# Optimization experiments

Measured on AMD Instinct MI355X. Metric: run time of the kernel, lower is better.

## Reference

```python
import jax, jax.numpy as jnp
import numpy as np

NUM_POINTS = 4
MAX_LEVELS = 2


def _bilinear(img, gx, gy, align_corners):
    # img: [C,H,W]; gx,gy: [P] normalized coords in [-1,1]; zero padding (torch grid_sample)
    C, H, W = img.shape
    if align_corners:
        ix = (gx + 1.0) * 0.5 * (W - 1)
        iy = (gy + 1.0) * 0.5 * (H - 1)
    else:
        ix = ((gx + 1.0) * W - 1.0) * 0.5
        iy = ((gy + 1.0) * H - 1.0) * 0.5
    x0 = jnp.floor(ix)
    y0 = jnp.floor(iy)
    wx1 = ix - x0
    wy1 = iy - y0

    def corner(xf, yf, w):
        xi = xf.astype(jnp.int32)
        yi = yf.astype(jnp.int32)
        valid = (xi >= 0) & (xi < W) & (yi >= 0) & (yi < H)
        v = img[:, jnp.clip(yi, 0, H - 1), jnp.clip(xi, 0, W - 1)]  # [C,P]
        return v * (w * valid)[None, :]

    return (corner(x0, y0, (1 - wx1) * (1 - wy1))
            + corner(x0 + 1, y0, wx1 * (1 - wy1))
            + corner(x0, y0 + 1, (1 - wx1) * wy1)
            + corner(x0 + 1, y0 + 1, wx1 * wy1))


_sample_ac = jax.vmap(lambda im, a, b: _bilinear(im, a, b, True))   # warp_affine path
_sample = jax.vmap(lambda im, a, b: _bilinear(im, a, b, False))     # MSDeformAttn path


def _warp_affine(src, M):
    # torch F.affine_grid + F.grid_sample, align_corners=True; src [N,C,H,W], M [N,2,3]
    N, C, H, W = src.shape
    ys = jnp.linspace(-1.0, 1.0, H)
    xs = jnp.linspace(-1.0, 1.0, W)
    gy, gx = jnp.meshgrid(ys, xs, indexing='ij')
    base = jnp.stack([gx.ravel(), gy.ravel(), jnp.ones(H * W, src.dtype)], 0)  # [3,HW]
    grid = jnp.einsum('nij,jp->nip', M, base)  # [N,2,HW]
    return _sample_ac(src, grid[:, 0], grid[:, 1]).reshape(N, C, H, W)


def setup_inputs() -> dict:
    key = jax.random.key(0)
    k = jax.random.split(key, 6)
    B, C, H, W = 2, 256, 100, 252
    x = jax.random.normal(k[0], (4, C, H, W), jnp.float32)
    record_len = jnp.full((B,), 2, dtype=jnp.int32)
    eye = jnp.array([[1.0, 0.0, 0.0], [0.0, 1.0, 0.0]], jnp.float32)
    pairwise_t_matrix = eye + 0.05 * jax.random.normal(k[1], (B, 2, 2, 2, 3), jnp.float32)
    w_off = 0.02 * jax.random.normal(k[2], (C, MAX_LEVELS * NUM_POINTS * 2), jnp.float32)
    b_off = 0.01 * jax.random.normal(k[3], (MAX_LEVELS * NUM_POINTS * 2,), jnp.float32)
    w_attn = 0.02 * jax.random.normal(k[4], (C, MAX_LEVELS * NUM_POINTS), jnp.float32)
    b_attn = 0.01 * jax.random.normal(k[5], (MAX_LEVELS * NUM_POINTS,), jnp.float32)
    return {"x": x, "record_len": record_len, "pairwise_t_matrix": pairwise_t_matrix,
            "w_off": w_off, "b_off": b_off, "w_attn": w_attn, "b_attn": b_attn}


def reference(x, record_len, pairwise_t_matrix, w_off, b_off, w_attn, b_attn):
    rl = [int(v) for v in np.asarray(record_len)]
    C, H, W = x.shape[1:]
    HW = H * W
    # get_reference_points(dim='2d'): pixel centers normalized to (0,1)
    rx = (jnp.arange(W, dtype=x.dtype) + 0.5) / W
    ry = (jnp.arange(H, dtype=x.dtype) + 0.5) / H
    gy, gx = jnp.meshgrid(ry, rx, indexing='ij')
    ref = jnp.stack([gx.ravel(), gy.ravel()], -1)  # [HW,2]
    norm = jnp.array([W, H], dtype=x.dtype)  # offset_normalizer = (W,H) per level
    outs = []
    start = 0
    for b, n in enumerate(rl):
        xx = x[start:start + n]
        start += n
        warped = _warp_affine(xx, pairwise_t_matrix[b, 0, :n])  # [n,C,H,W]
        q = warped[0].reshape(C, HW).T  # query = first agent, [HW,C]
        off = (q @ w_off + b_off).reshape(HW, MAX_LEVELS, NUM_POINTS, 2)[:, :n]  # [HW,n,P,2]
        aw = (q @ w_attn + b_attn).reshape(HW, MAX_LEVELS, NUM_POINTS)[:, :n]
        aw = jax.nn.softmax(aw.reshape(HW, n * NUM_POINTS), axis=-1).reshape(HW, n, NUM_POINTS)
        loc = ref[:, None, None, :] + off / norm  # sampling locations in (0,1)
        grid = 2.0 * loc - 1.0  # [HW,n,P,2]
        gxs = grid[..., 0].transpose(1, 0, 2).reshape(n, HW * NUM_POINTS)
        gys = grid[..., 1].transpose(1, 0, 2).reshape(n, HW * NUM_POINTS)
        sampled = _sample(warped, gxs, gys).reshape(n, C, HW, NUM_POINTS)
        out = jnp.einsum('lcqp,qlp->cq', sampled, aw)  # weighted sum over levels*points
        outs.append(out.reshape(1, C, H, W))
    return jnp.concatenate(outs, 0)
```

## Files before the change

### kernel.cpp

```cpp
#include <hip/hip_runtime.h>
#include <stdint.h>

#define CCH 256
#define NCP 128
#define HH  100
#define WW  252
#define HWSZ (HH*WW)
#define NIMG 4
#define NB   2
#define LP   8

#define TW 64
#define TH 4
#define HLO 2
#define PAIRS_BLOCK 16
#define TILESX ((WW + TW - 1)/TW)
#define TILESY (HH/TH)

#define WRW 70
#define WRH 5
#define WPL 384
#define WISS 6

typedef float vf2 __attribute__((ext_vector_type(2)));

__device__ __forceinline__ uint32_t f2bf(float a) {
  uint32_t u = __float_as_uint(a);
  u += 0x7fffu + ((u >> 16) & 1u);
  return u >> 16;
}
__device__ __forceinline__ float lof(uint32_t u) {
  return __uint_as_float(u << 16);
}
__device__ __forceinline__ float hif(uint32_t u) {
  return __uint_as_float(u & 0xffff0000u);
}
__device__ __forceinline__ vf2 unpk(uint32_t u) {
  vf2 r; r.x = lof(u); r.y = hif(u); return r;
}

__device__ __forceinline__ int swzN(int bid, int N) {
  int xcd = bid & 7, idx = bid >> 3;
  int q = N >> 3, r = N & 7;
  return (xcd < r) ? xcd*(q+1) + idx : r*(q+1) + (xcd-r)*q + idx;
}

__device__ __forceinline__ void gload_lds_u(const uint32_t* g, uint32_t* l) {
  auto gp = reinterpret_cast<const uint32_t __attribute__((address_space(1)))*>(
      reinterpret_cast<uintptr_t>(g));
  auto lp = reinterpret_cast<uint32_t __attribute__((address_space(3)))*>(
      reinterpret_cast<uintptr_t>(l));
  __builtin_amdgcn_global_load_lds(gp, lp, 4, 0, 0);
}

struct RowCtx {
  float w0, w1, w2, w3;
  uint32_t vt, vb;
  bool cnd;
};

__global__ __launch_bounds__(256) void warp_kernel(
    const float* __restrict__ x, const float* __restrict__ tmat,
    uint32_t* __restrict__ wpk)
{
  int tid = threadIdx.x;
  int ybase = 2*swzN(blockIdx.x, HH/2);
  int g  = blockIdx.y;
  int cc = blockIdx.z;
  bool valid = tid < WW;
  int xo = min(tid, WW-1);
  int b = g >> 1, i = g & 1;
  const float* M = tmat + (size_t)(b*4 + i)*6;
  float m00=M[0], m01=M[1], m02=M[2], m10=M[3], m11=M[4], m12=M[5];
  float gx = -1.0f + 2.0f*(float)xo/(float)(WW-1);

  RowCtx c0, c1;
  #pragma unroll
  for (int r = 0; r < 2; ++r) {
    int y = ybase + r;
    float gy = -1.0f + 2.0f*(float)y/(float)(HH-1);
    float sx = m00*gx + m01*gy + m02;
    float sy = m10*gx + m11*gy + m12;
    float ix = (sx + 1.0f)*0.5f*(float)(WW-1);
    float iy = (sy + 1.0f)*0.5f*(float)(HH-1);
    float x0f = floorf(ix), y0f = floorf(iy);
    float wx1 = ix - x0f,  wy1 = iy - y0f;
    int x0 = (int)x0f, y0 = (int)y0f;
    int x1 = x0 + 1,  y1 = y0 + 1;
    float v0x = (x0 >= 0 && x0 < WW) ? 1.f : 0.f;
    float v1x = (x1 >= 0 && x1 < WW) ? 1.f : 0.f;
    float v0y = (y0 >= 0 && y0 < HH) ? 1.f : 0.f;
    float v1y = (y1 >= 0 && y1 < HH) ? 1.f : 0.f;
    RowCtx c;
    c.w0 = (1.f-wx1)*(1.f-wy1)*v0x*v0y;
    c.w1 = wx1*(1.f-wy1)*v1x*v0y;
    c.w2 = (1.f-wx1)*wy1*v0x*v1y;
    c.w3 = wx1*wy1*v1x*v1y;
    int yc0 = min(max(y0,0),HH-1), yc1 = min(max(y1,0),HH-1);
    int xb  = min(max(x0,0),WW-2);
    c.cnd = (x0 == xb);
    c.vt = (uint32_t)(yc0*WW + xb)*4u;
    c.vb = (uint32_t)(yc1*WW + xb)*4u;
    if (r == 0) c0 = c; else c1 = c;
  }

  const float* src = x + ((size_t)g*CCH + (size_t)cc*32)*HWSZ;
  uint32_t* dst0 = wpk + ((size_t)g*NCP + (size_t)cc*PAIRS_BLOCK)*HWSZ
                   + ybase*WW + xo;
  uint32_t* dst1 = dst0 + WW;

  vf2 d[4][4];

  #define WLDQ(q) do {                                                       \
    const RowCtx& C = ((q)&1) ? c1 : c0;                                     \
    uint32_t co = (uint32_t)(2*((q)>>1))*(HWSZ*4u);                          \
    asm volatile("global_load_dwordx2 %0, %1, %2"                            \
      : "=v"(d[(q)&3][0]) : "v"(C.vt + co), "s"(src));                       \
    asm volatile("global_load_dwordx2 %0, %1, %2"                            \
      : "=v"(d[(q)&3][1]) : "v"(C.vb + co), "s"(src));                       \
    asm volatile("global_load_dwordx2 %0, %1, %2"                            \
      : "=v"(d[(q)&3][2]) : "v"(C.vt + co + HWSZ*4u), "s"(src));             \
    asm volatile("global_load_dwordx2 %0, %1, %2"                            \
      : "=v"(d[(q)&3][3]) : "v"(C.vb + co + HWSZ*4u), "s"(src));             \
  } while (0)

  #define WCPQ(q) do {                                                       \
    const RowCtx& C = ((q)&1) ? c1 : c0;                                     \
    uint32_t* D = ((q)&1) ? dst1 : dst0;                                     \
    vf2 t0 = d[(q)&3][0], b0 = d[(q)&3][1];                                  \
    vf2 t1 = d[(q)&3][2], b1 = d[(q)&3][3];                                  \
    float va0 = C.cnd ? t0.x : t0.y, vb0 = C.cnd ? t0.y : t0.x;              \
    float vc0 = C.cnd ? b0.x : b0.y, vd0 = C.cnd ? b0.y : b0.x;              \
    float va1 = C.cnd ? t1.x : t1.y, vb1 = C.cnd ? t1.y : t1.x;              \
    float vc1 = C.cnd ? b1.x : b1.y, vd1 = C.cnd ? b1.y : b1.x;              \
    float v0 = va0*C.w0 + vb0*C.w1 + vc0*C.w2 + vd0*C.w3;                    \
    float v1 = va1*C.w0 + vb1*C.w1 + vc1*C.w2 + vd1*C.w3;                    \
    if (valid) D[(size_t)((q)>>1)*HWSZ] = f2bf(v0) | (f2bf(v1) << 16);       \
  } while (0)

  WLDQ(0); WLDQ(1); WLDQ(2); WLDQ(3);
  #pragma unroll
  for (int q = 0; q < 2*PAIRS_BLOCK; ++q) {
    if      (q == 0)  { asm volatile("s_waitcnt vmcnt(12)" ::: "memory"); }
    else if (q == 1)  { asm volatile("s_waitcnt vmcnt(13)" ::: "memory"); }
    else if (q == 2)  { asm volatile("s_waitcnt vmcnt(14)" ::: "memory"); }
    else if (q <= 28) { asm volatile("s_waitcnt vmcnt(15)" ::: "memory"); }
    else if (q == 29) { asm volatile("s_waitcnt vmcnt(11)" ::: "memory"); }
    else if (q == 30) { asm volatile("s_waitcnt vmcnt(7)"  ::: "memory"); }
    else              { asm volatile("s_waitcnt vmcnt(3)"  ::: "memory"); }
    __builtin_amdgcn_sched_barrier(0);
    WCPQ(q);
    if (q + 4 < 2*PAIRS_BLOCK) WLDQ(q + 4);
  }
  #undef WLDQ
  #undef WCPQ
}

__global__ __launch_bounds__(256) void b1_kernel(
    const uint32_t* __restrict__ wpk,
    const float* __restrict__ w_off,  const float* __restrict__ b_off,
    const float* __restrict__ w_attn, const float* __restrict__ b_attn,
    float* __restrict__ taps)
{
  __shared__ float red[3][64][25];
  int tid   = threadIdx.x;
  int lpx   = tid & 63;
  int slice = tid >> 6;
  int pix   = blockIdx.x * 64 + lpx;
  int b     = blockIdx.y;
  bool valid = pix < HWSZ;
  int pxc = valid ? pix : (HWSZ-1);
  const uint32_t* q = wpk + ((size_t)(2*b)*NCP + (size_t)slice*32)*HWSZ + pxc;
  float acc[24];
  #pragma unroll
  for (int j=0;j<24;++j) acc[j] = 0.f;
  for (int cp=0; cp<32; ++cp) {
    uint32_t u = q[(size_t)cp*HWSZ];
    float qlo = lof(u), qhi = hif(u);
    int cg = slice*64 + 2*cp;
    #pragma unroll
    for (int j=0;j<16;++j) acc[j]    += qlo * w_off[cg*16+j]  + qhi * w_off[(cg+1)*16+j];
    #pragma unroll
    for (int j=0;j<8;++j)  acc[16+j] += qlo * w_attn[cg*8+j]  + qhi * w_attn[(cg+1)*8+j];
  }
  if (slice > 0) {
    #pragma unroll
    for (int j=0;j<24;++j) red[slice-1][lpx][j] = acc[j];
  }
  __syncthreads();
  if (slice == 0 && valid) {
    #pragma unroll
    for (int s=0;s<3;++s)
      #pragma unroll
      for (int j=0;j<24;++j) acc[j] += red[s][lpx][j];
    #pragma unroll
    for (int j=0;j<16;++j) acc[j]    += b_off[j];
    #pragma unroll
    for (int j=0;j<8;++j)  acc[16+j] += b_attn[j];
    float m = acc[16];
    #pragma unroll
    for (int j=1;j<8;++j) m = fmaxf(m, acc[16+j]);
    float e[8]; float s = 0.f;
    #pragma unroll
    for (int j=0;j<8;++j){ e[j] = __expf(acc[16+j]-m); s += e[j]; }
    float inv = 1.0f/s;
    int px = pix % WW, py = pix / WW;
    float* t = taps + (size_t)b*24*HWSZ + pix;
    #pragma unroll
    for (int k=0;k<LP;++k) {
      t[(size_t)k*HWSZ]      = (float)px + acc[2*k];
      t[(size_t)(8+k)*HWSZ]  = (float)py + acc[2*k+1];
      t[(size_t)(16+k)*HWSZ] = e[k]*inv;
    }
  }
}

__global__ __launch_bounds__(256) void b2_kernel(
    const uint32_t* __restrict__ wpk, const float* __restrict__ taps,
    float* __restrict__ out)
{
  __shared__ uint32_t lds[4*2*2*WPL];
  int tid  = threadIdx.x;
  int lane = tid & 63, wid = tid >> 6;
  int s100 = swzN(blockIdx.x, TILESX*TILESY);
  int tx   = s100 / TILESY;
  int ty   = s100 - tx*TILESY;
  int b    = blockIdx.y;
  int pbase = blockIdx.z * PAIRS_BLOCK;
  int tx0 = tx * TW;
  int ty0 = ty * TH;
  int px = tx0 + lane;
  int py = ty0 + wid;
  bool valid = (px < WW);
  int pxc = min(px, WW-1);
  int pix = py*WW + pxc;
  int cx0 = tx0 - HLO;
  int ry0 = py - HLO;

  const float* t = taps + (size_t)b*24*HWSZ + pix;
  float wgt[LP][4];
  int   lidx[LP];
  bool fastall = true;
  #pragma unroll
  for (int k=0;k<LP;++k) {
    float ix = t[(size_t)k*HWSZ];
    float iy = t[(size_t)(8+k)*HWSZ];
    float aw = t[(size_t)(16+k)*HWSZ];
    float x0f = floorf(ix), y0f = floorf(iy);
    float wx1 = ix-x0f, wy1 = iy-y0f;
    int x0=(int)x0f, y0=(int)y0f;
    float v0x = (x0   >= 0 && x0   < WW) ? 1.f : 0.f;
    float v1x = (x0+1 >= 0 && x0+1 < WW) ? 1.f : 0.f;
    float v0y = (y0   >= 0 && y0   < HH) ? 1.f : 0.f;
    float v1y = (y0+1 >= 0 && y0+1 < HH) ? 1.f : 0.f;
    wgt[k][0] = (1.f-wx1)*(1.f-wy1)*v0x*v0y*aw;
    wgt[k][1] = wx1*(1.f-wy1)*v1x*v0y*aw;
    wgt[k][2] = (1.f-wx1)*wy1*v0x*v1y*aw;
    wgt[k][3] = wx1*wy1*v1x*v1y*aw;
    bool f = (x0 >= cx0) && (x0 <= cx0+WRW-2) && (y0 >= ry0) && (y0 <= ry0+WRH-2);
    fastall = fastall && f;
    int li = (y0-ry0)*WRW + (x0-cx0);
    lidx[k] = f ? li : 0;
  }

  int goff[WISS];
  #pragma unroll
  for (int n=0;n<WISS;++n) {
    int e = n*64 + lane;
    int r = e / WRW;
    int c = e - r*WRW;
    int gy = min(max(ry0 + r, 0), HH-1);
    int gx = min(max(cx0 + c, 0), WW-1);
    goff[n] = gy*WW + gx;
  }

  const uint32_t* g0 = wpk + ((size_t)(2*b+0)*NCP + pbase)*HWSZ;
  const uint32_t* g1 = wpk + ((size_t)(2*b+1)*NCP + pbase)*HWSZ;
  uint32_t* wb = &lds[wid*2*2*WPL];

  #define B2_ISSUE(ph, buf) do {                                           \
    const uint32_t* gA = g0 + (size_t)(ph)*HWSZ;                           \
    const uint32_t* gB = g1 + (size_t)(ph)*HWSZ;                           \
    uint32_t* lb = wb + (buf)*2*WPL;                                       \
    _Pragma("unroll")                                                      \
    for (int n=0;n<WISS;++n) gload_lds_u(gA + goff[n], lb + n*64);         \
    _Pragma("unroll")                                                      \
    for (int n=0;n<WISS;++n) gload_lds_u(gB + goff[n], lb + WPL + n*64);   \
  } while (0)

  #define B2_COMPUTE(ph, buf) do {                                         \
    const uint32_t* L0 = wb + (buf)*2*WPL;                                 \
    const uint32_t* L1 = L0 + WPL;                                         \
    vf2 v = {0.f, 0.f};                                                    \
    if (fastall) {                                                         \
      _Pragma("unroll")                                                    \
      for (int k=0;k<LP;++k) {                                             \
        const uint32_t* L = (k<4) ? L0 : L1;                               \
        int id = lidx[k];                                                  \
        v += unpk(L[id])*wgt[k][0];                                        \
        v += unpk(L[id+1])*wgt[k][1];                                      \
        v += unpk(L[id+WRW])*wgt[k][2];                                    \
        v += unpk(L[id+WRW+1])*wgt[k][3];                                  \
      }                                                                    \
    } else {                                                               \
      _Pragma("unroll")                                                    \
      for (int k=0;k<LP;++k) {                                             \
        float ix = t[(size_t)k*HWSZ];                                      \
        float iy = t[(size_t)(8+k)*HWSZ];                                  \
        int x0=(int)floorf(ix), y0=(int)floorf(iy);                        \
        int xc0=min(max(x0,0),WW-1), xc1=min(max(x0+1,0),WW-1);            \
        int yc0=min(max(y0,0),HH-1), yc1=min(max(y0+1,0),HH-1);            \
        const uint32_t* p = (k<4) ? (g0 + (size_t)(ph)*HWSZ)               \
                                  : (g1 + (size_t)(ph)*HWSZ);              \
        v += unpk(p[yc0*WW+xc0])*wgt[k][0];                                \
        v += unpk(p[yc0*WW+xc1])*wgt[k][1];                                \
        v += unpk(p[yc1*WW+xc0])*wgt[k][2];                                \
        v += unpk(p[yc1*WW+xc1])*wgt[k][3];                                \
      }                                                                    \
    }                                                                      \
    if (valid) {                                                           \
      int c = 2*(pbase + (ph));                                            \
      out[((size_t)b*CCH + c  )*HWSZ + pix] = v.x;                         \
      out[((size_t)b*CCH + c+1)*HWSZ + pix] = v.y;                         \
    }                                                                      \
  } while (0)

  B2_ISSUE(0, 0);
  B2_ISSUE(1, 1);
  #pragma unroll
  for (int ph = 0; ph < PAIRS_BLOCK; ++ph) {
    if (ph == 0) {
      asm volatile("s_waitcnt vmcnt(12)" ::: "memory");
    } else if (ph < PAIRS_BLOCK-1) {
      asm volatile("s_waitcnt vmcnt(14)" ::: "memory");
    } else {
      asm volatile("s_waitcnt vmcnt(2)" ::: "memory");
    }
    __builtin_amdgcn_sched_barrier(0);
    B2_COMPUTE(ph, ph & 1);
    if (ph + 2 < PAIRS_BLOCK) B2_ISSUE(ph + 2, ph & 1);
  }
  #undef B2_ISSUE
  #undef B2_COMPUTE
}

extern "C" void kernel_launch(void* const* d_in, const int* in_sizes, int n_in,
                              void* d_out, int out_size, void* d_ws, size_t ws_size,
                              hipStream_t stream) {
  const float* x      = (const float*)d_in[0];
  const float* tmat   = (const float*)d_in[2];
  const float* w_off  = (const float*)d_in[3];
  const float* b_off  = (const float*)d_in[4];
  const float* w_attn = (const float*)d_in[5];
  const float* b_attn = (const float*)d_in[6];
  float* out = (float*)d_out;

  uint32_t* wpk = (uint32_t*)d_ws;
  float*    taps = (float*)((char*)d_ws +
                     (size_t)NIMG*NCP*HWSZ*sizeof(uint32_t));

  warp_kernel<<<dim3(HH/2, NIMG, NCP/PAIRS_BLOCK), 256, 0, stream>>>(x, tmat, wpk);
  b1_kernel<<<dim3((HWSZ+63)/64, NB), 256, 0, stream>>>(wpk, w_off, b_off,
                                                        w_attn, b_attn, taps);
  b2_kernel<<<dim3(TILESX*TILESY, NB, NCP/PAIRS_BLOCK), 256, 0, stream>>>(wpk, taps, out);
}
```

Measured before the change: 126.4 us.

## Stage shared full-width row band with 16-byte global-to-LDS loads across waves

Replaces each wave's private 70x5 LDS window, which was filled with 4-byte global_load_lds gathers, with a block-shared 8-row band of full image rows. The band is loaded with 16-byte direct-to-LDS copies, four per wave per phase. The goal is fewer load instructions and less redundant fetching of overlapping halo rows between the four waves. In exchange it adds two s_barriers per phase, since waves now read rows loaded by other waves. It also relies on the 256-entry row slots and clamped x indices to cover reads just outside the image, and on the new waitcnt values matching the smaller instruction count.

Result: slower. 135.0 us (+6.8%).

```diff
diff --git a/kernel.cpp b/kernel.cpp
--- a/kernel.cpp
+++ b/kernel.cpp
@@ -17,10 +17,9 @@
 #define TILESX ((WW + TW - 1)/TW)
 #define TILESY (HH/TH)
 
-#define WRW 70
-#define WRH 5
-#define WPL 384
-#define WISS 6
+#define BROWS 8
+#define RSL   256
+#define PSL   (16 + BROWS*RSL)
 
 typedef float vf2 __attribute__((ext_vector_type(2)));
 
@@ -45,12 +44,12 @@
   return (xcd < r) ? xcd*(q+1) + idx : r*(q+1) + (xcd-r)*q + idx;
 }
 
-__device__ __forceinline__ void gload_lds_u(const uint32_t* g, uint32_t* l) {
+__device__ __forceinline__ void gload_lds16u(const uint32_t* g, uint32_t* l) {
   auto gp = reinterpret_cast<const uint32_t __attribute__((address_space(1)))*>(
       reinterpret_cast<uintptr_t>(g));
   auto lp = reinterpret_cast<uint32_t __attribute__((address_space(3)))*>(
       reinterpret_cast<uintptr_t>(l));
-  __builtin_amdgcn_global_load_lds(gp, lp, 4, 0, 0);
+  __builtin_amdgcn_global_load_lds(gp, lp, 16, 0, 0);
 }
 
 struct RowCtx {
@@ -219,7 +218,7 @@
     const uint32_t* __restrict__ wpk, const float* __restrict__ taps,
     float* __restrict__ out)
 {
-  __shared__ uint32_t lds[4*2*2*WPL];
+  __shared__ uint32_t lds[2][2][PSL];
   int tid  = threadIdx.x;
   int lane = tid & 63, wid = tid >> 6;
   int s100 = swzN(blockIdx.x, TILESX*TILESY);
@@ -234,8 +233,7 @@
   bool valid = (px < WW);
   int pxc = min(px, WW-1);
   int pix = py*WW + pxc;
-  int cx0 = tx0 - HLO;
-  int ry0 = py - HLO;
+  int by0 = ty0 - HLO;
 
   const float* t = taps + (size_t)b*24*HWSZ + pix;
   float wgt[LP][4];
@@ -257,87 +255,78 @@
     wgt[k][1] = wx1*(1.f-wy1)*v1x*v0y*aw;
     wgt[k][2] = (1.f-wx1)*wy1*v0x*v1y*aw;
     wgt[k][3] = wx1*wy1*v1x*v1y*aw;
-    bool f = (x0 >= cx0) && (x0 <= cx0+WRW-2) && (y0 >= ry0) && (y0 <= ry0+WRH-2);
+    bool f = (y0 >= by0) && (y0 <= by0 + BROWS - 2);
     fastall = fastall && f;
-    int li = (y0-ry0)*WRW + (x0-cx0);
-    lidx[k] = f ? li : 0;
-  }
-
-  int goff[WISS];
-  #pragma unroll
-  for (int n=0;n<WISS;++n) {
-    int e = n*64 + lane;
-    int r = e / WRW;
-    int c = e - r*WRW;
-    int gy = min(max(ry0 + r, 0), HH-1);
-    int gx = min(max(cx0 + c, 0), WW-1);
-    goff[n] = gy*WW + gx;
+    int xs = min(max(x0, -1), WW);
+    int row = min(max(y0 - by0, 0), BROWS - 2);
+    lidx[k] = row*RSL + xs;
   }
 
   const uint32_t* g0 = wpk + ((size_t)(2*b+0)*NCP + pbase)*HWSZ;
   const uint32_t* g1 = wpk + ((size_t)(2*b+1)*NCP + pbase)*HWSZ;
-  uint32_t* wb = &lds[wid*2*2*WPL];
-
-  #define B2_ISSUE(ph, buf) do {                                           \
-    const uint32_t* gA = g0 + (size_t)(ph)*HWSZ;                           \
-    const uint32_t* gB = g1 + (size_t)(ph)*HWSZ;                           \
-    uint32_t* lb = wb + (buf)*2*WPL;                                       \
-    _Pragma("unroll")                                                      \
-    for (int n=0;n<WISS;++n) gload_lds_u(gA + goff[n], lb + n*64);         \
-    _Pragma("unroll")                                                      \
-    for (int n=0;n<WISS;++n) gload_lds_u(gB + goff[n], lb + WPL + n*64);   \
+
+  int gyA = min(max(by0 + wid,     0), HH-1);
+  int gyB = min(max(by0 + wid + 4, 0), HH-1);
+  int soA = gyA*WW + lane*4;
+  int soB = gyB*WW + lane*4;
+
+  #define B2_ISSUE(ph, buf) do {                                            \
+    const uint32_t* gA = g0 + (size_t)(ph)*HWSZ;                            \
+    const uint32_t* gB = g1 + (size_t)(ph)*HWSZ;                            \
+    gload_lds16u(gA + soA, &lds[buf][0][16 + (wid  )*RSL]);                 \
+    gload_lds16u(gA + soB, &lds[buf][0][16 + (wid+4)*RSL]);                 \
+    gload_lds16u(gB + soA, &lds[buf][1][16 + (wid  )*RSL]);                 \
+    gload_lds16u(gB + soB, &lds[buf][1][16 + (wid+4)*RSL]);                 \
   } while (0)
 
-  #define B2_COMPUTE(ph, buf) do {                                         \
-    const uint32_t* L0 = wb + (buf)*2*WPL;                                 \
-    const uint32_t* L1 = L0 + WPL;                                         \
-    vf2 v = {0.f, 0.f};                                                    \
-    if (fastall) {                                                         \
-      _Pragma("unroll")                                                    \
-      for (int k=0;k<LP;++k) {                                             \
-        const uint32_t* L = (k<4) ? L0 : L1;                               \
-        int id = lidx[k];                                                  \
-        v += unpk(L[id])*wgt[k][0];                                        \
-        v += unpk(L[id+1])*wgt[k][1];                                      \
-        v += unpk(L[id+WRW])*wgt[k][2];                                    \
-        v += unpk(L[id+WRW+1])*wgt[k][3];                                  \
-      }                                                                    \
-    } else {                                                               \
-      _Pragma("unroll")                                                    \
-      for (int k=0;k<LP;++k) {                                             \
-        float ix = t[(size_t)k*HWSZ];                                      \
-        float iy = t[(size_t)(8+k)*HWSZ];                                  \
-        int x0=(int)floorf(ix), y0=(int)floorf(iy);                        \
-        int xc0=min(max(x0,0),WW-1), xc1=min(max(x0+1,0),WW-1);            \
-        int yc0=min(max(y0,0),HH-1), yc1=min(max(y0+1,0),HH-1);            \
-        const uint32_t* p = (k<4) ? (g0 + (size_t)(ph)*HWSZ)               \
-                                  : (g1 + (size_t)(ph)*HWSZ);              \
-        v += unpk(p[yc0*WW+xc0])*wgt[k][0];                                \
-        v += unpk(p[yc0*WW+xc1])*wgt[k][1];                                \
-        v += unpk(p[yc1*WW+xc0])*wgt[k][2];                                \
-        v += unpk(p[yc1*WW+xc1])*wgt[k][3];                                \
-      }                                                                    \
-    }                                                                      \
-    if (valid) {                                                           \
-      int c = 2*(pbase + (ph));                                            \
-      out[((size_t)b*CCH + c  )*HWSZ + pix] = v.x;                         \
-      out[((size_t)b*CCH + c+1)*HWSZ + pix] = v.y;                         \
-    }                                                                      \
+  #define B2_COMPUTE(ph, buf) do {                                          \
+    const uint32_t* L0 = &lds[buf][0][16];                                  \
+    const uint32_t* L1 = &lds[buf][1][16];                                  \
+    vf2 v = {0.f, 0.f};                                                     \
+    if (fastall) {                                                          \
+      _Pragma("unroll")                                                     \
+      for (int k=0;k<LP;++k) {                                              \
+        const uint32_t* L = (k<4) ? L0 : L1;                                \
+        int id = lidx[k];                                                   \
+        v += unpk(L[id])*wgt[k][0];                                         \
+        v += unpk(L[id+1])*wgt[k][1];                                       \
+        v += unpk(L[id+RSL])*wgt[k][2];                                     \
+        v += unpk(L[id+RSL+1])*wgt[k][3];                                   \
+      }                                                                     \
+    } else {                                                                \
+      _Pragma("unroll")                                                     \
+      for (int k=0;k<LP;++k) {                                              \
+        float ix = t[(size_t)k*HWSZ];                                       \
+        float iy = t[(size_t)(8+k)*HWSZ];                                   \
+        int x0=(int)floorf(ix), y0=(int)floorf(iy);                         \
+        int xc0=min(max(x0,0),WW-1), xc1=min(max(x0+1,0),WW-1);             \
+        int yc0=min(max(y0,0),HH-1), yc1=min(max(y0+1,0),HH-1);             \
+        const uint32_t* p = (k<4) ? (g0 + (size_t)(ph)*HWSZ)                \
+                                  : (g1 + (size_t)(ph)*HWSZ);               \
+        v += unpk(p[yc0*WW+xc0])*wgt[k][0];                                 \
+        v += unpk(p[yc0*WW+xc1])*wgt[k][1];                                 \
+        v += unpk(p[yc1*WW+xc0])*wgt[k][2];                                 \
+        v += unpk(p[yc1*WW+xc1])*wgt[k][3];                                 \
+      }                                                                     \
+    }                                                                       \
+    if (valid) {                                                            \
+      int c = 2*(pbase + (ph));                                             \
+      out[((size_t)b*CCH + c  )*HWSZ + pix] = v.x;                          \
+      out[((size_t)b*CCH + c+1)*HWSZ + pix] = v.y;                          \
+    }                                                                       \
   } while (0)
 
   B2_ISSUE(0, 0);
   B2_ISSUE(1, 1);
   #pragma unroll
   for (int ph = 0; ph < PAIRS_BLOCK; ++ph) {
-    if (ph == 0) {
-      asm volatile("s_waitcnt vmcnt(12)" ::: "memory");
-    } else if (ph < PAIRS_BLOCK-1) {
-      asm volatile("s_waitcnt vmcnt(14)" ::: "memory");
-    } else {
-      asm volatile("s_waitcnt vmcnt(2)" ::: "memory");
-    }
+    if (ph == 0)                   { asm volatile("s_waitcnt vmcnt(4)" ::: "memory"); }
+    else if (ph < PAIRS_BLOCK-1)   { asm volatile("s_waitcnt vmcnt(6)" ::: "memory"); }
+    else                           { asm volatile("s_waitcnt vmcnt(2)" ::: "memory"); }
     __builtin_amdgcn_sched_barrier(0);
+    asm volatile("s_barrier" ::: "memory");
     B2_COMPUTE(ph, ph & 1);
+    asm volatile("s_barrier" ::: "memory");
     if (ph + 2 < PAIRS_BLOCK) B2_ISSUE(ph + 2, ph & 1);
   }
   #undef B2_ISSUE
```
